# Kernel optimization log

Measured on AMD Instinct MI355X. Metric: run time of the kernel, lower is better.

## Reference

```python
import jax, jax.numpy as jnp
import numpy as np
import math

D_MODEL = 1024
NHEADS = 16
HEAD_DIM = D_MODEL // NHEADS
SEQLEN = 2048
BS = 4


def setup_inputs() -> dict:
    key = jax.random.key(0)
    kq, kk, kv, kwq, kwk, kwv, kwo = jax.random.split(key, 7)
    q = jax.random.normal(kq, (SEQLEN, BS, D_MODEL), dtype=jnp.float32)
    k = jax.random.normal(kk, (SEQLEN, BS, D_MODEL), dtype=jnp.float32)
    v = jax.random.normal(kv, (SEQLEN, BS, D_MODEL), dtype=jnp.float32)
    # proper RoPE table: (seq, head_dim//2, 2) with (cos, sin)
    inv_freq = 1.0 / (10000.0 ** (np.arange(0, HEAD_DIM, 2, dtype=np.float32) / HEAD_DIM))
    angles = np.arange(SEQLEN, dtype=np.float32)[:, None] * inv_freq[None, :]
    freqs_cis = jnp.asarray(np.stack([np.cos(angles), np.sin(angles)], axis=-1))
    scale = 1.0 / math.sqrt(D_MODEL)
    wq = jax.random.normal(kwq, (D_MODEL, D_MODEL), dtype=jnp.float32) * scale
    wk = jax.random.normal(kwk, (D_MODEL, D_MODEL), dtype=jnp.float32) * scale
    wv = jax.random.normal(kwv, (D_MODEL, D_MODEL), dtype=jnp.float32) * scale
    wo = jax.random.normal(kwo, (D_MODEL, D_MODEL), dtype=jnp.float32) * scale
    return {"q": q, "k": k, "v": v, "freqs_cis": freqs_cis,
            "wq": wq, "wk": wk, "wv": wv, "wo": wo}


def _apply_rope(x, fc):
    # x: (L, B, H, hd) -> complex rotation on (hd//2, 2) pairs
    L, B, H, hd = x.shape
    x2 = x.reshape(L, B, H, hd // 2, 2)
    fc = fc[:L].reshape(L, 1, 1, hd // 2, 2)  # broadcast over batch, heads
    real = x2[..., 0] * fc[..., 0] - x2[..., 1] * fc[..., 1]
    imag = x2[..., 1] * fc[..., 0] + x2[..., 0] * fc[..., 1]
    return jnp.stack([real, imag], axis=-1).reshape(L, B, H, hd)


def reference(q, k, v, freqs_cis, wq, wk, wv, wo):
    S, B, D = q.shape
    L = k.shape[0]
    H, hd = NHEADS, HEAD_DIM
    # torch Linear: y = x @ W^T, W: (out, in)
    xq = jnp.einsum('sbd,ed->sbe', q, wq).reshape(S, B, H, hd)
    xk = jnp.einsum('lbd,ed->lbe', k, wk).reshape(L, B, H, hd)
    xv = jnp.einsum('lbd,ed->lbe', v, wv).reshape(L, B, H, hd)
    xq = _apply_rope(xq, freqs_cis)
    xk = _apply_rope(xk, freqs_cis)
    # scores: (B, H, S, L)
    scores = jnp.einsum('sbhd,lbhd->bhsl', xq, xk) / math.sqrt(hd)
    probs = jax.nn.softmax(scores.astype(jnp.float32), axis=-1).astype(xq.dtype)
    out = jnp.einsum('bhsl,lbhd->sbhd', probs, xv).reshape(S, B, H * hd)
    return jnp.einsum('sbe,de->sbd', out, wo)
```

## Files before the change

### kernel.cpp

```cpp
#include <hip/hip_runtime.h>
#include <hip/hip_bf16.h>

#define S_LEN   2048
#define BATCH   4
#define DMODEL  1024
#define NHEADS  16
#define HDIM    64
#define MROWS   (S_LEN * BATCH)

#define NE_ 8388608u
#define WE_ 1048576u

typedef unsigned int uint32;
typedef __attribute__((ext_vector_type(8))) short bf16x8;
typedef __attribute__((ext_vector_type(4))) float f32x4;

__device__ __forceinline__ ushort f2bf(float f) {
    uint32 u = __float_as_uint(f);
    uint32 r = (u + 0x7FFFu + ((u >> 16) & 1u)) >> 16;
    return (ushort)r;
}

__device__ __forceinline__ uint32 pk_bf16(float a, float b) {
    uint32 r;
    asm("v_cvt_pk_bf16_f32 %0, %1, %2" : "=v"(r) : "v"(a), "v"(b));
    return r;
}

__device__ __forceinline__ float exp2_asm(float x) {
    float r;
    asm("v_exp_f32 %0, %1" : "=v"(r) : "v"(x));
    return r;
}

__device__ __forceinline__ void gl16(const ushort* g, ushort* l) {
    __builtin_amdgcn_global_load_lds(
        (const __attribute__((address_space(1))) unsigned int*)g,
        (__attribute__((address_space(3))) unsigned int*)l,
        16, 0, 0);
}

__global__ __launch_bounds__(256) void cvt_all(const float* __restrict__ q,
                                               const float* __restrict__ k,
                                               const float* __restrict__ v,
                                               const float* __restrict__ wq,
                                               const float* __restrict__ wk,
                                               const float* __restrict__ wv,
                                               const float* __restrict__ wo,
                                               ushort* __restrict__ ws) {
    int i = blockIdx.x * 256 + threadIdx.x;
    const float* src;
    ushort* dst;
    int j;
    if (i < 3 * 2097152) {
        int t = i >> 21;
        j = i & 2097151;
        src = (t == 0) ? q : (t == 1) ? k : v;
        dst = ws + (size_t)t * NE_;
    } else {
        int u2 = i - 3 * 2097152;
        int t = u2 >> 18;
        j = u2 & 262143;
        src = (t == 0) ? wq : (t == 1) ? wk : (t == 2) ? wv : wo;
        dst = ws + 3 * (size_t)NE_ + (size_t)t * WE_;
    }
    float4 f = ((const float4*)src)[j];
    ushort4 u;
    u.x = f2bf(f.x); u.y = f2bf(f.y); u.z = f2bf(f.z); u.w = f2bf(f.w);
    ((ushort4*)dst)[j] = u;
}

__global__ __launch_bounds__(256) void proj_gemm(const ushort* __restrict__ abase,
                                                 const ushort* __restrict__ wbase,
                                                 const float* __restrict__ FC,
                                                 ushort* __restrict__ Qh,
                                                 ushort* __restrict__ Kh,
                                                 ushort* __restrict__ Vt) {
    __shared__ __align__(16) ushort SMEM[18432];
    ushort* A_lds = SMEM;
    ushort* B_lds = SMEM + 8192;

    const int tid  = threadIdx.x;
    const int lane = tid & 63;
    const int wvx  = tid >> 6;
    const int wm   = wvx >> 1, wn = wvx & 1;
    const int quad = lane >> 4, l16 = lane & 15;
    const int pid   = (gridDim.x == 512) ? 2 : (blockIdx.x >> 9);
    const int local = blockIdx.x & 511;
    const int m0 = (local >> 3) * 128;
    const int n0 = (local & 7) * 128;

    const ushort* A = abase + (size_t)pid * NE_;
    const ushort* W = wbase + (size_t)pid * WE_;

    const int srow = tid >> 2;
    const int scol = (tid & 3) * 8;

    f32x4 acc[4][4] = {};

    for (int k0 = 0; k0 < 1024; k0 += 32) {
        __syncthreads();
        gl16(&A[(size_t)(m0 + srow) * 1024 + k0 + scol],      &A_lds[tid * 8]);
        gl16(&A[(size_t)(m0 + 64 + srow) * 1024 + k0 + scol], &A_lds[2048 + tid * 8]);
        gl16(&W[(size_t)(n0 + srow) * 1024 + k0 + scol],      &B_lds[tid * 8]);
        gl16(&W[(size_t)(n0 + 64 + srow) * 1024 + k0 + scol], &B_lds[2048 + tid * 8]);
        __syncthreads();

        const ushort* Ab = &A_lds[(wm * 64 + l16) * 32 + quad * 8];
        const ushort* Bb = &B_lds[(wn * 64 + l16) * 32 + quad * 8];
        bf16x8 af[4], bfr[4];
#pragma unroll
        for (int i = 0; i < 4; ++i) af[i]  = *(const bf16x8*)(Ab + i * 512);
#pragma unroll
        for (int i = 0; i < 4; ++i) bfr[i] = *(const bf16x8*)(Bb + i * 512);
#pragma unroll
        for (int im = 0; im < 4; ++im)
#pragma unroll
            for (int in = 0; in < 4; ++in)
                acc[im][in] = __builtin_amdgcn_mfma_f32_16x16x32_bf16(
                    af[im], bfr[in], acc[im][in], 0, 0, 0);
    }

    const int s0 = (local >> 3) * 32;
    const int h0 = n0 >> 6;
    __syncthreads();

    if (pid < 2) {
        ushort* outb    = pid ? Kh : Qh;
        const float osc = pid ? 1.0f : 0.18033688011111793f;
#pragma unroll
        for (int im = 0; im < 4; ++im) {
            int mbase = m0 + wm * 64 + im * 16 + quad * 4;
            int s = mbase >> 2;
            int rho_base = wn * 32 + wm * 16 + im * 4 + quad;
#pragma unroll
            for (int in = 0; in < 4; ++in) {
                int dd = in * 16 + l16;
                float2 cs = *(const float2*)&FC[s * 64 + (dd & ~1)];
                float sgn = (dd & 1) ? 1.0f : -1.0f;
#pragma unroll
                for (int rr = 0; rr < 4; ++rr) {
                    float vv = acc[im][in][rr];
                    float pp = __shfl_xor(vv, 1, 64);
                    float ov = (vv * cs.x + sgn * pp * cs.y) * osc;
                    SMEM[(rr * 64 + rho_base) * 68 + dd] = f2bf(ov);
                }
            }
        }
        __syncthreads();
        {
            int rho = tid;
            int b = rho >> 6, hbit = (rho >> 5) & 1, srl = rho & 31;
            const uint2* src = (const uint2*)&SMEM[rho * 68];
            ushort* dst = &outb[((size_t)((b * 16 + h0 + hbit) * 2048) + s0 + srl) * 64];
#pragma unroll
            for (int j = 0; j < 8; ++j) {
                uint2 a0 = src[2 * j];
                uint2 a1 = src[2 * j + 1];
                ((uint4*)dst)[j] = make_uint4(a0.x, a0.y, a1.x, a1.y);
            }
        }
    } else {
#pragma unroll
        for (int im = 0; im < 4; ++im) {
            int pr = im * 8 + wm * 4 + quad;
#pragma unroll
            for (int in = 0; in < 4; ++in) {
                int ep = wn * 64 + in * 16 + l16;
#pragma unroll
                for (int rr = 0; rr < 4; ++rr)
                    SMEM[(rr * 128 + ep) * 36 + pr] = f2bf(acc[im][in][rr]);
            }
        }
        __syncthreads();
#pragma unroll
        for (int ppp = 0; ppp < 2; ++ppp) {
            int r = tid + ppp * 256;
            int b = r >> 7, ep = r & 127;
            int hh = h0 + (ep >> 6), dd = ep & 63;
            const uint2* src = (const uint2*)&SMEM[r * 36];
            ushort* dst = &Vt[((size_t)((b * 16 + hh) * 64 + dd)) * 2048 + s0];
#pragma unroll
            for (int j = 0; j < 4; ++j) {
                uint2 a0 = src[2 * j];
                uint2 a1 = src[2 * j + 1];
                ((uint4*)dst)[j] = make_uint4(a0.x, a0.y, a1.x, a1.y);
            }
        }
    }
}

__global__ __launch_bounds__(256) void out_gemm(const ushort* __restrict__ A,
                                                const ushort* __restrict__ W,
                                                float* __restrict__ outf) {
    __shared__ __align__(16) ushort A_lds[128 * 32];
    __shared__ __align__(16) ushort B_lds[128 * 32];

    const int tid  = threadIdx.x;
    const int lane = tid & 63;
    const int wvx  = tid >> 6;
    const int wm   = wvx >> 1, wn = wvx & 1;
    const int quad = lane >> 4, l16 = lane & 15;
    const int m0 = (blockIdx.x >> 3) * 128;
    const int n0 = (blockIdx.x & 7) * 128;

    const int srow = tid >> 2;
    const int scol = (tid & 3) * 8;

    f32x4 acc[4][4] = {};

    for (int k0 = 0; k0 < 1024; k0 += 32) {
        __syncthreads();
        gl16(&A[(size_t)(m0 + srow) * 1024 + k0 + scol],      &A_lds[tid * 8]);
        gl16(&A[(size_t)(m0 + 64 + srow) * 1024 + k0 + scol], &A_lds[2048 + tid * 8]);
        gl16(&W[(size_t)(n0 + srow) * 1024 + k0 + scol],      &B_lds[tid * 8]);
        gl16(&W[(size_t)(n0 + 64 + srow) * 1024 + k0 + scol], &B_lds[2048 + tid * 8]);
        __syncthreads();

        const ushort* Ab = &A_lds[(wm * 64 + l16) * 32 + quad * 8];
        const ushort* Bb = &B_lds[(wn * 64 + l16) * 32 + quad * 8];
        bf16x8 af[4], bfr[4];
#pragma unroll
        for (int i = 0; i < 4; ++i) af[i]  = *(const bf16x8*)(Ab + i * 512);
#pragma unroll
        for (int i = 0; i < 4; ++i) bfr[i] = *(const bf16x8*)(Bb + i * 512);
#pragma unroll
        for (int im = 0; im < 4; ++im)
#pragma unroll
            for (int in = 0; in < 4; ++in)
                acc[im][in] = __builtin_amdgcn_mfma_f32_16x16x32_bf16(
                    af[im], bfr[in], acc[im][in], 0, 0, 0);
    }

#pragma unroll
    for (int im = 0; im < 4; ++im) {
        int mbase = m0 + wm * 64 + im * 16 + quad * 4;
#pragma unroll
        for (int in = 0; in < 4; ++in) {
            int e = n0 + wn * 64 + in * 16 + l16;
#pragma unroll
            for (int rr = 0; rr < 4; ++rr)
                outf[(size_t)(mbase + rr) * 1024 + e] = acc[im][in][rr];
        }
    }
}

__global__ __launch_bounds__(256, 4) void attn_mfma(const ushort* __restrict__ Qb,
                                                    const ushort* __restrict__ Kb,
                                                    const ushort* __restrict__ Vt,
                                                    ushort* __restrict__ Ob) {
    __shared__ __align__(16) ushort KV[16384];

    const int tid  = threadIdx.x;
    const int lane = tid & 63;
    const int wv   = tid >> 6;
    const int quad = lane >> 4;
    const int l16  = lane & 15;

    const int bid  = blockIdx.x;
    const int xcd  = bid & 7;
    const int slot = bid >> 3;
    const int head = ((slot >> 4) << 3) | xcd;
    const int qt   = slot & 15;

    const int q0   = qt * 128 + wv * 32;
    const size_t hb = (size_t)head * (S_LEN * HDIM);

    bf16x8 qf[2][2];
#pragma unroll
    for (int im = 0; im < 2; ++im)
#pragma unroll
        for (int kk = 0; kk < 2; ++kk)
            qf[im][kk] = *(const bf16x8*)
                &Qb[hb + (size_t)(q0 + im * 16 + l16) * HDIM + kk * 32 + quad * 8];

    f32x4 o[2][4] = {};
    float lsum[2] = {0.f, 0.f};

    const int srow = tid >> 3;
    const int scol = (((tid & 7) ^ (srow & 7)) * 8);
    const int sx   = (l16 & 7) * 8;

    {
        ushort* dst = &KV[0];
        gl16(&Kb[hb + (size_t)(srow) * HDIM + scol],        dst + tid * 8);
        gl16(&Kb[hb + (size_t)(32 + srow) * HDIM + scol],   dst + 2048 + tid * 8);
        gl16(&Vt[hb + (size_t)srow * S_LEN + scol],         dst + 4096 + tid * 8);
        gl16(&Vt[hb + (size_t)(32 + srow) * S_LEN + scol],  dst + 4096 + 2048 + tid * 8);
    }

#pragma unroll 2
    for (int t = 0; t < 32; ++t) {
        if (t < 31) {
            ushort* dst = &KV[((t + 1) & 1) * 8192];
            const int kc = (t + 1) * 64;
            gl16(&Kb[hb + (size_t)(kc + srow) * HDIM + scol],      dst + tid * 8);
            gl16(&Kb[hb + (size_t)(kc + 32 + srow) * HDIM + scol], dst + 2048 + tid * 8);
            gl16(&Vt[hb + (size_t)srow * S_LEN + kc + scol],       dst + 4096 + tid * 8);
            gl16(&Vt[hb + (size_t)(32 + srow) * S_LEN + kc + scol], dst + 4096 + 2048 + tid * 8);
            asm volatile("s_waitcnt vmcnt(4)" ::: "memory");
        } else {
            asm volatile("s_waitcnt vmcnt(0)" ::: "memory");
        }
        __builtin_amdgcn_s_barrier();
        __builtin_amdgcn_sched_barrier(0);

        const ushort* Ksub = &KV[(t & 1) * 8192];
        const ushort* Vsub = Ksub + 4096;

        f32x4 st[2][4] = {};
        __builtin_amdgcn_s_setprio(1);
#pragma unroll
        for (int nt = 0; nt < 4; ++nt) {
            bf16x8 kf0 = *(const bf16x8*)&Ksub[(nt * 16 + l16) * 64 + ((quad * 8) ^ sx)];
            bf16x8 kf1 = *(const bf16x8*)&Ksub[(nt * 16 + l16) * 64 + ((32 + quad * 8) ^ sx)];
#pragma unroll
            for (int im = 0; im < 2; ++im) {
                st[im][nt] = __builtin_amdgcn_mfma_f32_16x16x32_bf16(
                    kf0, qf[im][0], st[im][nt], 0, 0, 0);
                st[im][nt] = __builtin_amdgcn_mfma_f32_16x16x32_bf16(
                    kf1, qf[im][1], st[im][nt], 0, 0, 0);
            }
        }
        __builtin_amdgcn_s_setprio(0);

        union { uint32 d[16]; bf16x8 v[4]; } P;
#pragma unroll
        for (int im = 0; im < 2; ++im) {
            float ls = 0.f;
#pragma unroll
            for (int nt = 0; nt < 4; ++nt) {
                float p0 = exp2_asm(st[im][nt][0]);
                float p1 = exp2_asm(st[im][nt][1]);
                float p2 = exp2_asm(st[im][nt][2]);
                float p3 = exp2_asm(st[im][nt][3]);
                ls += (p0 + p1) + (p2 + p3);
                P.d[im * 8 + nt * 2]     = pk_bf16(p0, p1);
                P.d[im * 8 + nt * 2 + 1] = pk_bf16(p2, p3);
            }
            lsum[im] += ls;
        }

        __builtin_amdgcn_s_setprio(1);
#pragma unroll
        for (int dt = 0; dt < 4; ++dt) {
            bf16x8 vf0 = *(const bf16x8*)&Vsub[(dt * 16 + l16) * 64 + ((quad * 8) ^ sx)];
            bf16x8 vf1 = *(const bf16x8*)&Vsub[(dt * 16 + l16) * 64 + ((32 + quad * 8) ^ sx)];
#pragma unroll
            for (int im = 0; im < 2; ++im) {
                o[im][dt] = __builtin_amdgcn_mfma_f32_16x16x32_bf16(
                    vf0, P.v[im * 2], o[im][dt], 0, 0, 0);
                o[im][dt] = __builtin_amdgcn_mfma_f32_16x16x32_bf16(
                    vf1, P.v[im * 2 + 1], o[im][dt], 0, 0, 0);
            }
        }
        __builtin_amdgcn_s_setprio(0);

        __builtin_amdgcn_s_barrier();
        __builtin_amdgcn_sched_barrier(0);
    }

#pragma unroll
    for (int im = 0; im < 2; ++im) {
        lsum[im] += __shfl_xor(lsum[im], 16, 64);
        lsum[im] += __shfl_xor(lsum[im], 32, 64);
    }

    ushort* Est = &KV[wv * 2048];
#pragma unroll
    for (int im = 0; im < 2; ++im) {
        float inv = 1.0f / lsum[im];
#pragma unroll
        for (int dt = 0; dt < 4; ++dt) {
            uint2 w;
            w.x = pk_bf16(o[im][dt][0] * inv, o[im][dt][1] * inv);
            w.y = pk_bf16(o[im][dt][2] * inv, o[im][dt][3] * inv);
            *(uint2*)&Est[(im * 16 + l16) * 64 + dt * 16 + quad * 4] = w;
        }
    }
    __syncthreads();

    const int row  = lane >> 1, half = lane & 1;
    const int b = head >> 4, h = head & 15;
    const size_t ob = (size_t)((q0 + row) * BATCH + b) * 1024 + h * 64 + half * 32;
#pragma unroll
    for (int e = 0; e < 4; ++e) {
        bf16x8 t = *(const bf16x8*)&Est[row * 64 + half * 32 + e * 8];
        *(bf16x8*)&Ob[ob + e * 8] = t;
    }
}

extern "C" void kernel_launch(void* const* d_in, const int* in_sizes, int n_in,
                              void* d_out, int out_size, void* d_ws, size_t ws_size,
                              hipStream_t stream) {
    const float* q   = (const float*)d_in[0];
    const float* k   = (const float*)d_in[1];
    const float* v   = (const float*)d_in[2];
    const float* fc  = (const float*)d_in[3];
    const float* wq  = (const float*)d_in[4];
    const float* wk  = (const float*)d_in[5];
    const float* wvp = (const float*)d_in[6];
    const float* wo  = (const float*)d_in[7];

    ushort* ws = (ushort*)d_ws;
    ushort* qb  = ws;
    ushort* kb  = ws + NE_;
    ushort* wqb = ws + 3 * (size_t)NE_;
    ushort* wob = wqb + 3 * (size_t)WE_;

    ushort* Qh = (ushort*)d_out;
    ushort* Kh = Qh + NE_;
    ushort* Vt = ws;
    ushort* R3 = ws + NE_;

    cvt_all<<<28672, 256, 0, stream>>>(q, k, v, wq, wk, wvp, wo, ws);

    proj_gemm<<<1024, 256, 0, stream>>>(qb, wqb, fc, Qh, Kh, Vt);

    proj_gemm<<<512, 256, 0, stream>>>(qb, wqb, fc, Qh, Kh, Vt);

    attn_mfma<<<1024, 256, 0, stream>>>(Qh, Kh, Vt, R3);

    out_gemm<<<512, 256, 0, stream>>>(R3, wob, (float*)d_out);
}
```

Measured before the change: 364.8 us.

## Double-buffer GEMM LDS loads, fuse QKV projections, write epilogue directly

Both projection and output GEMMs now double-buffer LDS tiles, prefetching the next K slice while MFMAs run on the current one, which removes one barrier per iteration. When the workspace is large enough, V^T goes to a separate buffer so the Q/K/V projections can run in a single 1536-block launch with interleaved block ordering. The LDS-staged epilogue transposes are replaced with direct scattered global stores, using a permuted position layout for V^T. This saves LDS round trips but makes the global writes less coalesced.

```diff
diff --git a/kernel.cpp b/kernel.cpp
--- a/kernel.cpp
+++ b/kernel.cpp
@@ -75,20 +75,34 @@
                                                  const float* __restrict__ FC,
                                                  ushort* __restrict__ Qh,
                                                  ushort* __restrict__ Kh,
-                                                 ushort* __restrict__ Vt) {
-    __shared__ __align__(16) ushort SMEM[18432];
-    ushort* A_lds = SMEM;
-    ushort* B_lds = SMEM + 8192;
+                                                 ushort* __restrict__ Vt,
+                                                 int mode) {
+    __shared__ __align__(16) ushort SM[16384];
 
     const int tid  = threadIdx.x;
     const int lane = tid & 63;
     const int wvx  = tid >> 6;
     const int wm   = wvx >> 1, wn = wvx & 1;
     const int quad = lane >> 4, l16 = lane & 15;
-    const int pid   = (gridDim.x == 512) ? 2 : (blockIdx.x >> 9);
-    const int local = blockIdx.x & 511;
-    const int m0 = (local >> 3) * 128;
-    const int n0 = (local & 7) * 128;
+
+    int pid, m_idx, n_idx;
+    if (mode == 0) {
+        int p = blockIdx.x % 24;
+        m_idx = blockIdx.x / 24;
+        pid   = p >> 3;
+        n_idx = p & 7;
+    } else if (mode == 1) {
+        pid   = blockIdx.x >> 9;
+        int local = blockIdx.x & 511;
+        m_idx = local >> 3;
+        n_idx = local & 7;
+    } else {
+        pid   = 2;
+        m_idx = blockIdx.x >> 3;
+        n_idx = blockIdx.x & 7;
+    }
+    const int m0 = m_idx * 128;
+    const int n0 = n_idx * 128;
 
     const ushort* A = abase + (size_t)pid * NE_;
     const ushort* W = wbase + (size_t)pid * WE_;
@@ -98,16 +112,29 @@
 
     f32x4 acc[4][4] = {};
 
-    for (int k0 = 0; k0 < 1024; k0 += 32) {
-        __syncthreads();
-        gl16(&A[(size_t)(m0 + srow) * 1024 + k0 + scol],      &A_lds[tid * 8]);
-        gl16(&A[(size_t)(m0 + 64 + srow) * 1024 + k0 + scol], &A_lds[2048 + tid * 8]);
-        gl16(&W[(size_t)(n0 + srow) * 1024 + k0 + scol],      &B_lds[tid * 8]);
-        gl16(&W[(size_t)(n0 + 64 + srow) * 1024 + k0 + scol], &B_lds[2048 + tid * 8]);
-        __syncthreads();
-
-        const ushort* Ab = &A_lds[(wm * 64 + l16) * 32 + quad * 8];
-        const ushort* Bb = &B_lds[(wn * 64 + l16) * 32 + quad * 8];
+    {
+        ushort* D = &SM[0];
+        gl16(&A[(size_t)(m0 + srow) * 1024 + scol],        D + tid * 8);
+        gl16(&A[(size_t)(m0 + 64 + srow) * 1024 + scol],   D + 2048 + tid * 8);
+        gl16(&W[(size_t)(n0 + srow) * 1024 + scol],        D + 4096 + tid * 8);
+        gl16(&W[(size_t)(n0 + 64 + srow) * 1024 + scol],   D + 6144 + tid * 8);
+    }
+    __syncthreads();
+
+#pragma unroll 2
+    for (int kt = 0; kt < 32; ++kt) {
+        const int cur = kt & 1;
+        if (kt < 31) {
+            const int kk = (kt + 1) * 32;
+            ushort* D = &SM[(cur ^ 1) * 8192];
+            gl16(&A[(size_t)(m0 + srow) * 1024 + kk + scol],      D + tid * 8);
+            gl16(&A[(size_t)(m0 + 64 + srow) * 1024 + kk + scol], D + 2048 + tid * 8);
+            gl16(&W[(size_t)(n0 + srow) * 1024 + kk + scol],      D + 4096 + tid * 8);
+            gl16(&W[(size_t)(n0 + 64 + srow) * 1024 + kk + scol], D + 6144 + tid * 8);
+        }
+
+        const ushort* Ab = &SM[cur * 8192 + (wm * 64 + l16) * 32 + quad * 8];
+        const ushort* Bb = &SM[cur * 8192 + 4096 + (wn * 64 + l16) * 32 + quad * 8];
         bf16x8 af[4], bfr[4];
 #pragma unroll
         for (int i = 0; i < 4; ++i) af[i]  = *(const bf16x8*)(Ab + i * 512);
@@ -119,11 +146,9 @@
             for (int in = 0; in < 4; ++in)
                 acc[im][in] = __builtin_amdgcn_mfma_f32_16x16x32_bf16(
                     af[im], bfr[in], acc[im][in], 0, 0, 0);
-    }
-
-    const int s0 = (local >> 3) * 32;
-    const int h0 = n0 >> 6;
-    __syncthreads();
+
+        __syncthreads();
+    }
 
     if (pid < 2) {
         ushort* outb    = pid ? Kh : Qh;
@@ -132,10 +157,10 @@
         for (int im = 0; im < 4; ++im) {
             int mbase = m0 + wm * 64 + im * 16 + quad * 4;
             int s = mbase >> 2;
-            int rho_base = wn * 32 + wm * 16 + im * 4 + quad;
 #pragma unroll
             for (int in = 0; in < 4; ++in) {
-                int dd = in * 16 + l16;
+                int e = n0 + wn * 64 + in * 16 + l16;
+                int h = e >> 6, dd = e & 63;
                 float2 cs = *(const float2*)&FC[s * 64 + (dd & ~1)];
                 float sgn = (dd & 1) ? 1.0f : -1.0f;
 #pragma unroll
@@ -143,48 +168,28 @@
                     float vv = acc[im][in][rr];
                     float pp = __shfl_xor(vv, 1, 64);
                     float ov = (vv * cs.x + sgn * pp * cs.y) * osc;
-                    SMEM[(rr * 64 + rho_base) * 68 + dd] = f2bf(ov);
+                    outb[((size_t)(rr * NHEADS + h) * S_LEN + s) * HDIM + dd] = f2bf(ov);
                 }
             }
         }
-        __syncthreads();
-        {
-            int rho = tid;
-            int b = rho >> 6, hbit = (rho >> 5) & 1, srl = rho & 31;
-            const uint2* src = (const uint2*)&SMEM[rho * 68];
-            ushort* dst = &outb[((size_t)((b * 16 + h0 + hbit) * 2048) + s0 + srl) * 64];
-#pragma unroll
-            for (int j = 0; j < 8; ++j) {
-                uint2 a0 = src[2 * j];
-                uint2 a1 = src[2 * j + 1];
-                ((uint4*)dst)[j] = make_uint4(a0.x, a0.y, a1.x, a1.y);
-            }
-        }
     } else {
 #pragma unroll
         for (int im = 0; im < 4; ++im) {
-            int pr = im * 8 + wm * 4 + quad;
+            int mbase = m0 + wm * 64 + im * 16 + quad * 4;
+            int s = mbase >> 2;
+            int nt2 = (s >> 4) & 3;
+            int qd  = (s >> 2) & 3;
+            int r2  = s & 3;
+            int pos = (s & ~63) | ((nt2 >> 1) << 5) | (qd << 3) | ((nt2 & 1) << 2) | r2;
 #pragma unroll
             for (int in = 0; in < 4; ++in) {
-                int ep = wn * 64 + in * 16 + l16;
-#pragma unroll
-                for (int rr = 0; rr < 4; ++rr)
-                    SMEM[(rr * 128 + ep) * 36 + pr] = f2bf(acc[im][in][rr]);
-            }
-        }
-        __syncthreads();
-#pragma unroll
-        for (int ppp = 0; ppp < 2; ++ppp) {
-            int r = tid + ppp * 256;
-            int b = r >> 7, ep = r & 127;
-            int hh = h0 + (ep >> 6), dd = ep & 63;
-            const uint2* src = (const uint2*)&SMEM[r * 36];
-            ushort* dst = &Vt[((size_t)((b * 16 + hh) * 64 + dd)) * 2048 + s0];
-#pragma unroll
-            for (int j = 0; j < 4; ++j) {
-                uint2 a0 = src[2 * j];
-                uint2 a1 = src[2 * j + 1];
-                ((uint4*)dst)[j] = make_uint4(a0.x, a0.y, a1.x, a1.y);
+                int e = n0 + wn * 64 + in * 16 + l16;
+                int h = e >> 6, dd = e & 63;
+#pragma unroll
+                for (int rr = 0; rr < 4; ++rr) {
+                    Vt[((size_t)(rr * NHEADS + h) * HDIM + dd) * S_LEN + pos] =
+                        f2bf(acc[im][in][rr]);
+                }
             }
         }
     }
@@ -193,8 +198,7 @@
 __global__ __launch_bounds__(256) void out_gemm(const ushort* __restrict__ A,
                                                 const ushort* __restrict__ W,
                                                 float* __restrict__ outf) {
-    __shared__ __align__(16) ushort A_lds[128 * 32];
-    __shared__ __align__(16) ushort B_lds[128 * 32];
+    __shared__ __align__(16) ushort SM[16384];
 
     const int tid  = threadIdx.x;
     const int lane = tid & 63;
@@ -209,16 +213,29 @@
 
     f32x4 acc[4][4] = {};
 
-    for (int k0 = 0; k0 < 1024; k0 += 32) {
-        __syncthreads();
-        gl16(&A[(size_t)(m0 + srow) * 1024 + k0 + scol],      &A_lds[tid * 8]);
-        gl16(&A[(size_t)(m0 + 64 + srow) * 1024 + k0 + scol], &A_lds[2048 + tid * 8]);
-        gl16(&W[(size_t)(n0 + srow) * 1024 + k0 + scol],      &B_lds[tid * 8]);
-        gl16(&W[(size_t)(n0 + 64 + srow) * 1024 + k0 + scol], &B_lds[2048 + tid * 8]);
-        __syncthreads();
-
-        const ushort* Ab = &A_lds[(wm * 64 + l16) * 32 + quad * 8];
-        const ushort* Bb = &B_lds[(wn * 64 + l16) * 32 + quad * 8];
+    {
+        ushort* D = &SM[0];
+        gl16(&A[(size_t)(m0 + srow) * 1024 + scol],        D + tid * 8);
+        gl16(&A[(size_t)(m0 + 64 + srow) * 1024 + scol],   D + 2048 + tid * 8);
+        gl16(&W[(size_t)(n0 + srow) * 1024 + scol],        D + 4096 + tid * 8);
+        gl16(&W[(size_t)(n0 + 64 + srow) * 1024 + scol],   D + 6144 + tid * 8);
+    }
+    __syncthreads();
+
+#pragma unroll 2
+    for (int kt = 0; kt < 32; ++kt) {
+        const int cur = kt & 1;
+        if (kt < 31) {
+            const int kk = (kt + 1) * 32;
+            ushort* D = &SM[(cur ^ 1) * 8192];
+            gl16(&A[(size_t)(m0 + srow) * 1024 + kk + scol],      D + tid * 8);
+            gl16(&A[(size_t)(m0 + 64 + srow) * 1024 + kk + scol], D + 2048 + tid * 8);
+            gl16(&W[(size_t)(n0 + srow) * 1024 + kk + scol],      D + 4096 + tid * 8);
+            gl16(&W[(size_t)(n0 + 64 + srow) * 1024 + kk + scol], D + 6144 + tid * 8);
+        }
+
+        const ushort* Ab = &SM[cur * 8192 + (wm * 64 + l16) * 32 + quad * 8];
+        const ushort* Bb = &SM[cur * 8192 + 4096 + (wn * 64 + l16) * 32 + quad * 8];
         bf16x8 af[4], bfr[4];
 #pragma unroll
         for (int i = 0; i < 4; ++i) af[i]  = *(const bf16x8*)(Ab + i * 512);
@@ -230,6 +247,8 @@
             for (int in = 0; in < 4; ++in)
                 acc[im][in] = __builtin_amdgcn_mfma_f32_16x16x32_bf16(
                     af[im], bfr[in], acc[im][in], 0, 0, 0);
+
+        __syncthreads();
     }
 
 #pragma unroll
@@ -410,14 +429,20 @@
 
     ushort* Qh = (ushort*)d_out;
     ushort* Kh = Qh + NE_;
-    ushort* Vt = ws;
     ushort* R3 = ws + NE_;
 
+    const size_t baseElems = 3 * (size_t)NE_ + 4 * (size_t)WE_;
+    const bool   bigWs     = ws_size >= (baseElems + NE_) * sizeof(ushort);
+    ushort* Vt = bigWs ? (ws + baseElems) : qb;
+
     cvt_all<<<28672, 256, 0, stream>>>(q, k, v, wq, wk, wvp, wo, ws);
 
-    proj_gemm<<<1024, 256, 0, stream>>>(qb, wqb, fc, Qh, Kh, Vt);
-
-    proj_gemm<<<512, 256, 0, stream>>>(qb, wqb, fc, Qh, Kh, Vt);
+    if (bigWs) {
+        proj_gemm<<<1536, 256, 0, stream>>>(ws, wqb, fc, Qh, Kh, Vt, 0);
+    } else {
+        proj_gemm<<<1024, 256, 0, stream>>>(ws, wqb, fc, Qh, Kh, Vt, 1);
+        proj_gemm<<<512, 256, 0, stream>>>(ws, wqb, fc, Qh, Kh, Vt, 2);
+    }
 
     attn_mfma<<<1024, 256, 0, stream>>>(Qh, Kh, Vt, R3);
 
```

Result: no change. 368.6 us (+1.1%).
